# Kernel optimization log

Hardware: AMD Instinct MI355X
Metric: run time of the kernel (lower is better)

## Reference

```python
import jax, jax.numpy as jnp
import numpy as np

B, N, D, H, E = 4, 1024, 512, 8, 5
HD = D // H  # head_dim = 64


def _xavier(k, shape):
    fan_out, fan_in = shape
    s = (2.0 / (fan_in + fan_out)) ** 0.5
    return jax.random.normal(k, shape, jnp.float32) * s


def setup_inputs() -> dict:
    key = jax.random.key(0)
    ks = jax.random.split(key, 7)
    x = jax.random.normal(ks[0], (B, N, D), jnp.float32)
    edge_features = jax.random.normal(ks[1], (B, N, N, E), jnp.float32)
    node_mask = jax.random.randint(ks[2], (B, N), 0, 2).astype(bool)
    w_qkv = _xavier(ks[3], (3 * D, D))
    w_ep = _xavier(ks[4], (H, E))
    w_eg = _xavier(ks[5], (H, E))
    b_eg = jnp.zeros((H,), jnp.float32)
    w_proj = _xavier(ks[6], (D, D))
    b_proj = jnp.zeros((D,), jnp.float32)
    return {"x": x, "edge_features": edge_features, "node_mask": node_mask,
            "w_qkv": w_qkv, "w_ep": w_ep, "w_eg": w_eg, "b_eg": b_eg,
            "w_proj": w_proj, "b_proj": b_proj}


def reference(x, edge_features, node_mask, w_qkv, w_ep, w_eg, b_eg, w_proj, b_proj):
    b, n, d = x.shape
    scale = HD ** -0.5
    # qkv projection (torch Linear: y = x @ W^T), split into q,k,v (b,H,n,HD)
    qkv = (x @ w_qkv.T).reshape(b, n, 3, H, HD)
    qkv = jnp.transpose(qkv, (2, 0, 3, 1, 4))
    q, k, v = qkv[0], qkv[1], qkv[2]
    # attention scores (b,H,n,n)
    scores = jnp.einsum('bhnd,bhmd->bhnm', q, k) * scale
    # edge bias and sigmoid gate, (b,n,n,E) @ (E,H) -> (b,H,n,n)
    edge_bias = jnp.einsum('bnme,he->bhnm', edge_features, w_ep)
    edge_gates = jax.nn.sigmoid(
        jnp.einsum('bnme,he->bhnm', edge_features, w_eg) + b_eg[None, :, None, None])
    scores = scores + edge_gates * edge_bias
    # pairwise valid mask, broadcast over heads
    m = node_mask[:, None, :, None] & node_mask[:, None, None, :]  # (b,1,n,n)
    scores = jnp.where(m, scores, -jnp.inf)
    row_valid = jnp.any(m, axis=-1)  # (b,1,n)
    scores = jnp.where(row_valid[..., None], scores, 0.0)
    attn = jax.nn.softmax(scores, axis=-1)
    out = jnp.einsum('bhnm,bhmd->bhnd', attn, v)
    out = jnp.transpose(out, (0, 2, 1, 3)).reshape(b, n, d)
    return out @ w_proj.T + b_proj
```

## Files before the change

kernel.cpp:

```cpp
#include <hip/hip_runtime.h>
#include <hip/hip_bf16.h>

#define Bb 4
#define Nn 1024
#define Dd 512
#define Hh 8
#define Ee 5
#define HDd 64

typedef unsigned int u32_t;
typedef unsigned short u16_t;
typedef short s16x8 __attribute__((ext_vector_type(8)));
typedef float f32x4 __attribute__((ext_vector_type(4)));

#define MFMA(a, b, c) __builtin_amdgcn_mfma_f32_16x16x32_bf16((a), (b), (c), 0, 0, 0)

__device__ __forceinline__ u32_t pack32(float x) {
    u32_t u = __float_as_uint(x);
    u32_t hi = u & 0xffff0000u;
    float rem = x - __uint_as_float(hi);
    u32_t r = __float_as_uint(rem);
    u32_t lo = (r + 0x7fffu + ((r >> 16) & 1u)) >> 16;
    return hi | (lo & 0xffffu);
}

__device__ __forceinline__ void unpk8(uint4 A, uint4 B, s16x8& h, s16x8& l) {
    union { u16_t u[8]; s16x8 v; } H, L;
    u32_t a[8] = {A.x, A.y, A.z, A.w, B.x, B.y, B.z, B.w};
    #pragma unroll
    for (int i = 0; i < 8; i++) { H.u[i] = (u16_t)(a[i] >> 16); L.u[i] = (u16_t)(a[i] & 0xffffu); }
    h = H.v; l = L.v;
}

__device__ __forceinline__ void split4(uint4 A, uint2& hi, uint2& lo) {
    hi.x = (A.x >> 16) | (A.y & 0xffff0000u);
    hi.y = (A.z >> 16) | (A.w & 0xffff0000u);
    lo.x = (A.x & 0xffffu) | (A.y << 16);
    lo.y = (A.z & 0xffffu) | (A.w << 16);
}

__global__ __launch_bounds__(256) void prep_mask(const void* __restrict__ msk,
                                                 int* __restrict__ mw,
                                                 int* __restrict__ anyB) {
    __shared__ int notint;
    __shared__ int ab[Bb];
    const int tid = threadIdx.x;
    if (tid == 0) notint = 0;
    if (tid < Bb) ab[tid] = 0;
    __syncthreads();
    const u32_t* wp = (const u32_t*)msk;
    int bad = 0;
    for (int i = tid; i < 1024; i += 256) bad |= (wp[i] > 1u);
    if (bad) atomicOr(&notint, 1);
    __syncthreads();
    const int isbyte = notint;
    const unsigned char* bp = (const unsigned char*)msk;
    for (int i = tid; i < Bb * Nn; i += 256) {
        const int v = isbyte ? (bp[i] != 0) : (wp[i] != 0);
        mw[i] = v;
        if (v) atomicOr(&ab[i >> 10], 1);
    }
    __syncthreads();
    if (tid < Bb) anyB[tid] = ab[tid];
}

__global__ __launch_bounds__(256) void pack3(const float* __restrict__ x,
                                             const float* __restrict__ wq,
                                             const float* __restrict__ wpj,
                                             u32_t* __restrict__ xp,
                                             u32_t* __restrict__ wqp,
                                             u32_t* __restrict__ wpp) {
    const int gt = blockIdx.x * 256 + threadIdx.x;
    const int gs = gridDim.x * 256;
    const float4* xs = (const float4*)x;
    uint4* xd = (uint4*)xp;
    for (int i = gt; i < (Bb * Nn * Dd) / 4; i += gs) {
        float4 v = xs[i];
        xd[i] = make_uint4(pack32(v.x), pack32(v.y), pack32(v.z), pack32(v.w));
    }
    const float4* qs = (const float4*)wq;
    uint4* qd = (uint4*)wqp;
    for (int i = gt; i < (3 * Dd * Dd) / 4; i += gs) {
        float4 v = qs[i];
        qd[i] = make_uint4(pack32(v.x), pack32(v.y), pack32(v.z), pack32(v.w));
    }
    const float4* ps = (const float4*)wpj;
    uint4* pd = (uint4*)wpp;
    for (int i = gt; i < (Dd * Dd) / 4; i += gs) {
        float4 v = ps[i];
        pd[i] = make_uint4(pack32(v.x), pack32(v.y), pack32(v.z), pack32(v.w));
    }
}

__global__ __launch_bounds__(256) void qkv_mfma(const u32_t* __restrict__ xp,
                                                const u32_t* __restrict__ wp,
                                                u32_t* __restrict__ q32,
                                                u32_t* __restrict__ k32,
                                                u32_t* __restrict__ v32) {
    __shared__ __align__(16) u16_t Xh[64 * 72], Xl[64 * 72];
    __shared__ __align__(16) u16_t Wh[64 * 72], Wl[64 * 72];
    const int tid = threadIdx.x;
    const int wv = tid >> 6, lane = tid & 63, lm = lane & 15, quad = lane >> 4;
    const int m0 = blockIdx.y * 64, c0 = blockIdx.x * 64;
    const int row = tid >> 2, dq = tid & 3;
    const uint4* x4 = (const uint4*)xp;
    const uint4* w4 = (const uint4*)wp;

    f32x4 acc[4];
    #pragma unroll
    for (int nt = 0; nt < 4; nt++) acc[nt] = {0.f, 0.f, 0.f, 0.f};

    for (int kt = 0; kt < 8; kt++) {
        __syncthreads();
        #pragma unroll
        for (int t = 0; t < 4; t++) {
            const int cc = dq * 4 + t;
            uint4 A = x4[(size_t)(m0 + row) * 128 + kt * 16 + cc];
            uint2 hi, lo;
            split4(A, hi, lo);
            *(uint2*)&Xh[row * 72 + cc * 4] = hi;
            *(uint2*)&Xl[row * 72 + cc * 4] = lo;
            uint4 Bv = w4[(size_t)(c0 + row) * 128 + kt * 16 + cc];
            split4(Bv, hi, lo);
            *(uint2*)&Wh[row * 72 + cc * 4] = hi;
            *(uint2*)&Wl[row * 72 + cc * 4] = lo;
        }
        __syncthreads();
        s16x8 ah[2], al[2];
        #pragma unroll
        for (int ks = 0; ks < 2; ks++) {
            ah[ks] = *(const s16x8*)&Xh[(16 * wv + lm) * 72 + ks * 32 + quad * 8];
            al[ks] = *(const s16x8*)&Xl[(16 * wv + lm) * 72 + ks * 32 + quad * 8];
        }
        #pragma unroll
        for (int nt = 0; nt < 4; nt++) {
            #pragma unroll
            for (int ks = 0; ks < 2; ks++) {
                s16x8 bh = *(const s16x8*)&Wh[(16 * nt + lm) * 72 + ks * 32 + quad * 8];
                s16x8 bl = *(const s16x8*)&Wl[(16 * nt + lm) * 72 + ks * 32 + quad * 8];
                acc[nt] = MFMA(ah[ks], bh, acc[nt]);
                acc[nt] = MFMA(ah[ks], bl, acc[nt]);
                acc[nt] = MFMA(al[ks], bh, acc[nt]);
            }
        }
    }
    #pragma unroll
    for (int nt = 0; nt < 4; nt++) {
        const int c = c0 + 16 * nt + lm;
        const int s = c >> 9, hd = c & 511, h = hd >> 6, d = hd & 63;
        u32_t* dst = (s == 0) ? q32 : (s == 1) ? k32 : v32;
        #pragma unroll
        for (int r = 0; r < 4; r++) {
            const int m = m0 + 16 * wv + 4 * quad + r;
            const int b = m >> 10, n = m & (Nn - 1);
            dst[(((size_t)b * Hh + h) * Nn + n) * HDd + d] = pack32(acc[nt][r]);
        }
    }
}

__global__ __launch_bounds__(256, 2) void attn_mfma(const u32_t* __restrict__ q32,
                                                    const u32_t* __restrict__ k32,
                                                    const u32_t* __restrict__ v32,
                                                    const float* __restrict__ ef,
                                                    const int* __restrict__ mw,
                                                    const int* __restrict__ anyB,
                                                    const float* __restrict__ wep,
                                                    const float* __restrict__ weg,
                                                    const float* __restrict__ beg,
                                                    u32_t* __restrict__ aoutp) {
    __shared__ __align__(16) u16_t Qh[64 * 72], Ql[64 * 72];
    __shared__ __align__(16) char KP[18432];
    __shared__ __align__(16) u16_t VTh[64 * 88], VTl[64 * 88];
    u16_t* Kh = (u16_t*)KP;
    u16_t* Kl = Kh + 64 * 72;
    u32_t* Ppk = (u32_t*)KP;

    const int tid = threadIdx.x;
    const int wv = tid >> 6, lane = tid & 63, lm = lane & 15, quad = lane >> 4;
    const int i0 = blockIdx.x * 64;
    const int h  = blockIdx.y;
    const int b  = blockIdx.z;

    const float wp0 = wep[h*Ee+0], wp1 = wep[h*Ee+1], wp2 = wep[h*Ee+2],
                wp3 = wep[h*Ee+3], wp4 = wep[h*Ee+4];
    const float wg0 = weg[h*Ee+0], wg1 = weg[h*Ee+1], wg2 = weg[h*Ee+2],
                wg3 = weg[h*Ee+3], wg4 = weg[h*Ee+4];
    const float bgs = beg[h];

    const uint4* qg4 = (const uint4*)(q32 + (((size_t)b * Hh + h) * Nn + i0) * HDd);
    const uint4* kg4 = (const uint4*)(k32 + (((size_t)b * Hh + h) * Nn) * HDd);
    const uint4* vg4 = (const uint4*)(v32 + (((size_t)b * Hh + h) * Nn) * HDd);
    const int* mwB = mw + b * Nn;

    {
        const int row = tid >> 2, dq = tid & 3;
        #pragma unroll
        for (int t = 0; t < 4; t++) {
            const int cc = dq * 4 + t;
            uint4 A = qg4[row * 16 + cc];
            uint2 hi, lo;
            split4(A, hi, lo);
            *(uint2*)&Qh[row * 72 + cc * 4] = hi;
            *(uint2*)&Ql[row * 72 + cc * 4] = lo;
        }
    }

    const int anyb = anyB[b];
    int rv[4];
    float m_[4], l_[4];
    f32x4 accO[4];
    const float* efrow[4];
    #pragma unroll
    for (int r = 0; r < 4; r++) {
        const int i = i0 + 16 * wv + 4 * quad + r;
        rv[r] = anyb && mwB[i];
        m_[r] = -1e30f; l_[r] = 0.f;
        efrow[r] = ef + ((size_t)(b * Nn + i) * Nn + lm) * Ee;
    }
    #pragma unroll
    for (int dn = 0; dn < 4; dn++) accO[dn] = {0.f, 0.f, 0.f, 0.f};

    for (int jt = 0; jt < Nn / 64; jt++) {
        const int j0 = jt * 64;

        int mj[4];
        #pragma unroll
        for (int jn = 0; jn < 4; jn++) mj[jn] = mwB[j0 + 16 * jn + lm];
        float er[4][4][5];
        #pragma unroll
        for (int r = 0; r < 4; r++) {
            const float* pr = efrow[r] + (size_t)j0 * Ee;
            #pragma unroll
            for (int jn = 0; jn < 4; jn++) {
                #pragma unroll
                for (int e = 0; e < 5; e++) er[r][jn][e] = pr[jn * (16 * Ee) + e];
            }
        }

        __syncthreads();

        {
            const int row = tid >> 2, dq = tid & 3;
            #pragma unroll
            for (int t = 0; t < 4; t++) {
                const int cc = dq * 4 + t;
                uint4 A = kg4[(j0 + row) * 16 + cc];
                uint2 hi, lo;
                split4(A, hi, lo);
                *(uint2*)&Kh[row * 72 + cc * 4] = hi;
                *(uint2*)&Kl[row * 72 + cc * 4] = lo;
            }
        }
        {
            const int jg = tid >> 4, dc = tid & 15;
            u32_t r0[4], r1[4], r2[4], r3[4];
            uint4 A0 = vg4[(j0 + 4 * jg + 0) * 16 + dc];
            uint4 A1 = vg4[(j0 + 4 * jg + 1) * 16 + dc];
            uint4 A2 = vg4[(j0 + 4 * jg + 2) * 16 + dc];
            uint4 A3 = vg4[(j0 + 4 * jg + 3) * 16 + dc];
            r0[0]=A0.x; r0[1]=A0.y; r0[2]=A0.z; r0[3]=A0.w;
            r1[0]=A1.x; r1[1]=A1.y; r1[2]=A1.z; r1[3]=A1.w;
            r2[0]=A2.x; r2[1]=A2.y; r2[2]=A2.z; r2[3]=A2.w;
            r3[0]=A3.x; r3[1]=A3.y; r3[2]=A3.z; r3[3]=A3.w;
            #pragma unroll
            for (int c = 0; c < 4; c++) {
                const int d = 4 * dc + c;
                uint2 hi, lo;
                hi.x = (r0[c] >> 16) | (r1[c] & 0xffff0000u);
                hi.y = (r2[c] >> 16) | (r3[c] & 0xffff0000u);
                lo.x = (r0[c] & 0xffffu) | (r1[c] << 16);
                lo.y = (r2[c] & 0xffffu) | (r3[c] << 16);
                *(uint2*)&VTh[d * 88 + 4 * jg] = hi;
                *(uint2*)&VTl[d * 88 + 4 * jg] = lo;
            }
        }
        __syncthreads();

        s16x8 qh[2], ql[2];
        #pragma unroll
        for (int ks = 0; ks < 2; ks++) {
            qh[ks] = *(const s16x8*)&Qh[(16 * wv + lm) * 72 + ks * 32 + quad * 8];
            ql[ks] = *(const s16x8*)&Ql[(16 * wv + lm) * 72 + ks * 32 + quad * 8];
        }
        f32x4 S[4];
        #pragma unroll
        for (int jn = 0; jn < 4; jn++) {
            f32x4 s = {0.f, 0.f, 0.f, 0.f};
            #pragma unroll
            for (int ks = 0; ks < 2; ks++) {
                s16x8 bh = *(const s16x8*)&Kh[(16 * jn + lm) * 72 + ks * 32 + quad * 8];
                s16x8 bl = *(const s16x8*)&Kl[(16 * jn + lm) * 72 + ks * 32 + quad * 8];
                s = MFMA(qh[ks], bh, s);
                s = MFMA(qh[ks], bl, s);
                s = MFMA(ql[ks], bh, s);
            }
            S[jn] = s;
        }

        float pv[4][4];
        #pragma unroll
        for (int r = 0; r < 4; r++) {
            float sv[4];
            #pragma unroll
            for (int jn = 0; jn < 4; jn++) {
                const float e0 = er[r][jn][0], e1 = er[r][jn][1], e2 = er[r][jn][2],
                            e3 = er[r][jn][3], e4 = er[r][jn][4];
                const float bias = fmaf(e0, wp0, fmaf(e1, wp1, fmaf(e2, wp2, fmaf(e3, wp3, e4 * wp4))));
                const float gv = fmaf(e0, wg0, fmaf(e1, wg1, fmaf(e2, wg2, fmaf(e3, wg3, fmaf(e4, wg4, bgs)))));
                const float gate = __builtin_amdgcn_rcpf(1.f + __expf(-gv));
                const float val = fmaf(S[jn][r], 0.125f, gate * bias);
                sv[jn] = rv[r] ? (mj[jn] ? val : -1e30f) : 0.f;
            }
            float tmax = fmaxf(fmaxf(sv[0], sv[1]), fmaxf(sv[2], sv[3]));
            tmax = fmaxf(tmax, __shfl_xor(tmax, 1));
            tmax = fmaxf(tmax, __shfl_xor(tmax, 2));
            tmax = fmaxf(tmax, __shfl_xor(tmax, 4));
            tmax = fmaxf(tmax, __shfl_xor(tmax, 8));
            const float mnew = fmaxf(m_[r], tmax);
            const float alpha = __expf(m_[r] - mnew);
            float ps = 0.f;
            #pragma unroll
            for (int jn = 0; jn < 4; jn++) { pv[r][jn] = __expf(sv[jn] - mnew); ps += pv[r][jn]; }
            ps += __shfl_xor(ps, 1);
            ps += __shfl_xor(ps, 2);
            ps += __shfl_xor(ps, 4);
            ps += __shfl_xor(ps, 8);
            m_[r] = mnew;
            l_[r] = l_[r] * alpha + ps;
            #pragma unroll
            for (int dn = 0; dn < 4; dn++) accO[dn][r] *= alpha;
        }

        __syncthreads();
        #pragma unroll
        for (int r = 0; r < 4; r++)
            #pragma unroll
            for (int jn = 0; jn < 4; jn++)
                Ppk[(16 * wv + 4 * quad + r) * 68 + 16 * jn + lm] = pack32(pv[r][jn]);

        s16x8 ph[2], pl[2];
        #pragma unroll
        for (int ks2 = 0; ks2 < 2; ks2++) {
            const int off = (16 * wv + lm) * 68 + ks2 * 32 + quad * 8;
            uint4 A = *(const uint4*)&Ppk[off];
            uint4 B = *(const uint4*)&Ppk[off + 4];
            unpk8(A, B, ph[ks2], pl[ks2]);
        }
        #pragma unroll
        for (int dn = 0; dn < 4; dn++) {
            f32x4 c = accO[dn];
            #pragma unroll
            for (int ks2 = 0; ks2 < 2; ks2++) {
                s16x8 vh = *(const s16x8*)&VTh[(16 * dn + lm) * 88 + ks2 * 32 + quad * 8];
                s16x8 vl = *(const s16x8*)&VTl[(16 * dn + lm) * 88 + ks2 * 32 + quad * 8];
                c = MFMA(ph[ks2], vh, c);
                c = MFMA(ph[ks2], vl, c);
                c = MFMA(pl[ks2], vh, c);
            }
            accO[dn] = c;
        }
    }

    #pragma unroll
    for (int r = 0; r < 4; r++) {
        const int i = i0 + 16 * wv + 4 * quad + r;
        const float inv = __builtin_amdgcn_rcpf(l_[r]);
        #pragma unroll
        for (int dn = 0; dn < 4; dn++)
            aoutp[(size_t)(b * Nn + i) * Dd + h * HDd + 16 * dn + lm] = pack32(accO[dn][r] * inv);
    }
}

__global__ __launch_bounds__(256) void out_mfma(const u32_t* __restrict__ ap,
                                                const u32_t* __restrict__ wp,
                                                const float* __restrict__ bias,
                                                float* __restrict__ out) {
    __shared__ __align__(16) u16_t Xh[64 * 72], Xl[64 * 72];
    __shared__ __align__(16) u16_t Wh[64 * 72], Wl[64 * 72];
    const int tid = threadIdx.x;
    const int wv = tid >> 6, lane = tid & 63, lm = lane & 15, quad = lane >> 4;
    const int m0 = blockIdx.y * 64, c0 = blockIdx.x * 64;
    const int row = tid >> 2, dq = tid & 3;
    const uint4* a4 = (const uint4*)ap;
    const uint4* w4 = (const uint4*)wp;

    f32x4 acc[4];
    #pragma unroll
    for (int nt = 0; nt < 4; nt++) acc[nt] = {0.f, 0.f, 0.f, 0.f};

    for (int kt = 0; kt < 8; kt++) {
        __syncthreads();
        #pragma unroll
        for (int t = 0; t < 4; t++) {
            const int cc = dq * 4 + t;
            uint4 A = a4[(size_t)(m0 + row) * 128 + kt * 16 + cc];
            uint2 hi, lo;
            split4(A, hi, lo);
            *(uint2*)&Xh[row * 72 + cc * 4] = hi;
            *(uint2*)&Xl[row * 72 + cc * 4] = lo;
            uint4 Bv = w4[(size_t)(c0 + row) * 128 + kt * 16 + cc];
            split4(Bv, hi, lo);
            *(uint2*)&Wh[row * 72 + cc * 4] = hi;
            *(uint2*)&Wl[row * 72 + cc * 4] = lo;
        }
        __syncthreads();
        s16x8 ah[2], al[2];
        #pragma unroll
        for (int ks = 0; ks < 2; ks++) {
            ah[ks] = *(const s16x8*)&Xh[(16 * wv + lm) * 72 + ks * 32 + quad * 8];
            al[ks] = *(const s16x8*)&Xl[(16 * wv + lm) * 72 + ks * 32 + quad * 8];
        }
        #pragma unroll
        for (int nt = 0; nt < 4; nt++) {
            #pragma unroll
            for (int ks = 0; ks < 2; ks++) {
                s16x8 bh = *(const s16x8*)&Wh[(16 * nt + lm) * 72 + ks * 32 + quad * 8];
                s16x8 bl = *(const s16x8*)&Wl[(16 * nt + lm) * 72 + ks * 32 + quad * 8];
                acc[nt] = MFMA(ah[ks], bh, acc[nt]);
                acc[nt] = MFMA(ah[ks], bl, acc[nt]);
                acc[nt] = MFMA(al[ks], bh, acc[nt]);
            }
        }
    }
    #pragma unroll
    for (int nt = 0; nt < 4; nt++) {
        const int c = c0 + 16 * nt + lm;
        const float bc = bias[c];
        #pragma unroll
        for (int r = 0; r < 4; r++) {
            const int m = m0 + 16 * wv + 4 * quad + r;
            out[(size_t)m * Dd + c] = acc[nt][r] + bc;
        }
    }
}

extern "C" void kernel_launch(void* const* d_in, const int* in_sizes, int n_in,
                              void* d_out, int out_size, void* d_ws, size_t ws_size,
                              hipStream_t stream) {
    const float* x    = (const float*)d_in[0];
    const float* ef   = (const float*)d_in[1];
    const void*  msk  = d_in[2];
    const float* wqkv = (const float*)d_in[3];
    const float* wep  = (const float*)d_in[4];
    const float* weg  = (const float*)d_in[5];
    const float* beg  = (const float*)d_in[6];
    const float* wpj  = (const float*)d_in[7];
    const float* bpj  = (const float*)d_in[8];
    float* out = (float*)d_out;

    int* mw   = (int*)d_ws;
    int* anyB = mw + Bb * Nn;
    u32_t* q32 = (u32_t*)(anyB + 16);
    const size_t per = (size_t)Bb * Hh * Nn * HDd;
    u32_t* k32 = q32 + per;
    u32_t* v32 = k32 + per;
    u32_t* aop = v32 + per;
    u32_t* xp  = aop + (size_t)Bb * Nn * Dd;
    u32_t* wqp = xp + (size_t)Bb * Nn * Dd;
    u32_t* wpp = wqp + (size_t)3 * Dd * Dd;

    prep_mask<<<1, 256, 0, stream>>>(msk, mw, anyB);
    pack3<<<1024, 256, 0, stream>>>(x, wqkv, wpj, xp, wqp, wpp);
    qkv_mfma<<<dim3(24, 64), 256, 0, stream>>>(xp, wqp, q32, k32, v32);
    attn_mfma<<<dim3(Nn / 64, Hh, Bb), 256, 0, stream>>>(q32, k32, v32, ef, mw, anyB,
                                                         wep, weg, beg, aop);
    out_mfma<<<dim3(8, 64), 256, 0, stream>>>(aop, wpp, bpj, out);
}
```

Before: 310.9 us.

## Transpose score MFMA so edge features load as contiguous float4 per lane

The attention kernel now computes K·Qᵀ instead of Q·Kᵀ. Each lane then owns one query row and four consecutive key columns, so the edge-feature reads become contiguous float4 loads and the softmax row reductions run across quads instead of across 16 lanes. The P buffer gets its own XOR-swizzled shared-memory region, which removes one __syncthreads per tile at the cost of more LDS. Q fragments are hoisted out of the loop, and the staging loops in all three kernels use wider 16-byte LDS stores.

```diff
diff --git a/kernel.cpp b/kernel.cpp
--- a/kernel.cpp
+++ b/kernel.cpp
@@ -37,6 +37,16 @@
     hi.y = (A.z >> 16) | (A.w & 0xffff0000u);
     lo.x = (A.x & 0xffffu) | (A.y << 16);
     lo.y = (A.z & 0xffffu) | (A.w << 16);
+}
+
+__device__ __forceinline__ void stage16(uint4 A0, uint4 A1, uint4 A2, uint4 A3,
+                                        u16_t* dh, u16_t* dl) {
+    uint2 h0, l0, h1, l1, h2, l2, h3, l3;
+    split4(A0, h0, l0); split4(A1, h1, l1); split4(A2, h2, l2); split4(A3, h3, l3);
+    *(uint4*)(dh + 0) = make_uint4(h0.x, h0.y, h1.x, h1.y);
+    *(uint4*)(dh + 8) = make_uint4(h2.x, h2.y, h3.x, h3.y);
+    *(uint4*)(dl + 0) = make_uint4(l0.x, l0.y, l1.x, l1.y);
+    *(uint4*)(dl + 8) = make_uint4(l2.x, l2.y, l3.x, l3.y);
 }
 
 __global__ __launch_bounds__(256) void prep_mask(const void* __restrict__ msk,
@@ -112,18 +122,13 @@
 
     for (int kt = 0; kt < 8; kt++) {
         __syncthreads();
-        #pragma unroll
-        for (int t = 0; t < 4; t++) {
-            const int cc = dq * 4 + t;
-            uint4 A = x4[(size_t)(m0 + row) * 128 + kt * 16 + cc];
-            uint2 hi, lo;
-            split4(A, hi, lo);
-            *(uint2*)&Xh[row * 72 + cc * 4] = hi;
-            *(uint2*)&Xl[row * 72 + cc * 4] = lo;
-            uint4 Bv = w4[(size_t)(c0 + row) * 128 + kt * 16 + cc];
-            split4(Bv, hi, lo);
-            *(uint2*)&Wh[row * 72 + cc * 4] = hi;
-            *(uint2*)&Wl[row * 72 + cc * 4] = lo;
+        {
+            const size_t xb = (size_t)(m0 + row) * 128 + kt * 16 + dq * 4;
+            stage16(x4[xb + 0], x4[xb + 1], x4[xb + 2], x4[xb + 3],
+                    &Xh[row * 72 + dq * 16], &Xl[row * 72 + dq * 16]);
+            const size_t wb = (size_t)(c0 + row) * 128 + kt * 16 + dq * 4;
+            stage16(w4[wb + 0], w4[wb + 1], w4[wb + 2], w4[wb + 3],
+                    &Wh[row * 72 + dq * 16], &Wl[row * 72 + dq * 16]);
         }
         __syncthreads();
         s16x8 ah[2], al[2];
@@ -169,11 +174,9 @@
                                                     const float* __restrict__ beg,
                                                     u32_t* __restrict__ aoutp) {
     __shared__ __align__(16) u16_t Qh[64 * 72], Ql[64 * 72];
-    __shared__ __align__(16) char KP[18432];
+    __shared__ __align__(16) u16_t Kh[64 * 72], Kl[64 * 72];
     __shared__ __align__(16) u16_t VTh[64 * 88], VTl[64 * 88];
-    u16_t* Kh = (u16_t*)KP;
-    u16_t* Kl = Kh + 64 * 72;
-    u32_t* Ppk = (u32_t*)KP;
+    __shared__ __align__(16) u32_t Ppk[64 * 68];
 
     const int tid = threadIdx.x;
     const int wv = tid >> 6, lane = tid & 63, lm = lane & 15, quad = lane >> 4;
@@ -194,65 +197,51 @@
 
     {
         const int row = tid >> 2, dq = tid & 3;
-        #pragma unroll
-        for (int t = 0; t < 4; t++) {
-            const int cc = dq * 4 + t;
-            uint4 A = qg4[row * 16 + cc];
-            uint2 hi, lo;
-            split4(A, hi, lo);
-            *(uint2*)&Qh[row * 72 + cc * 4] = hi;
-            *(uint2*)&Ql[row * 72 + cc * 4] = lo;
-        }
+        const size_t qb = (size_t)row * 16 + dq * 4;
+        stage16(qg4[qb + 0], qg4[qb + 1], qg4[qb + 2], qg4[qb + 3],
+                &Qh[row * 72 + dq * 16], &Ql[row * 72 + dq * 16]);
+    }
+    __syncthreads();
+    s16x8 qh[2], ql[2];
+    #pragma unroll
+    for (int ks = 0; ks < 2; ks++) {
+        qh[ks] = *(const s16x8*)&Qh[(16 * wv + lm) * 72 + ks * 32 + quad * 8];
+        ql[ks] = *(const s16x8*)&Ql[(16 * wv + lm) * 72 + ks * 32 + quad * 8];
     }
 
     const int anyb = anyB[b];
-    int rv[4];
-    float m_[4], l_[4];
+    const int i_sm = i0 + 16 * wv + lm;
+    const int rvs = anyb && mwB[i_sm];
+    float m_ = -1e30f, l_ = 0.f;
     f32x4 accO[4];
-    const float* efrow[4];
-    #pragma unroll
-    for (int r = 0; r < 4; r++) {
-        const int i = i0 + 16 * wv + 4 * quad + r;
-        rv[r] = anyb && mwB[i];
-        m_[r] = -1e30f; l_[r] = 0.f;
-        efrow[r] = ef + ((size_t)(b * Nn + i) * Nn + lm) * Ee;
-    }
     #pragma unroll
     for (int dn = 0; dn < 4; dn++) accO[dn] = {0.f, 0.f, 0.f, 0.f};
+    const float* efL = ef + ((size_t)(b * Nn + i_sm) * Nn + 4 * quad) * Ee;
+    const int xk = 8 * (lm & 3);
 
     for (int jt = 0; jt < Nn / 64; jt++) {
         const int j0 = jt * 64;
 
-        int mj[4];
-        #pragma unroll
-        for (int jn = 0; jn < 4; jn++) mj[jn] = mwB[j0 + 16 * jn + lm];
-        float er[4][4][5];
-        #pragma unroll
-        for (int r = 0; r < 4; r++) {
-            const float* pr = efrow[r] + (size_t)j0 * Ee;
-            #pragma unroll
-            for (int jn = 0; jn < 4; jn++) {
-                #pragma unroll
-                for (int e = 0; e < 5; e++) er[r][jn][e] = pr[jn * (16 * Ee) + e];
-            }
+        int4 mj4[4];
+        float4 er4[4][5];
+        #pragma unroll
+        for (int jn = 0; jn < 4; jn++) {
+            mj4[jn] = *(const int4*)&mwB[j0 + 16 * jn + 4 * quad];
+            const float4* p4 = (const float4*)(efL + (size_t)(j0 + 16 * jn) * Ee);
+            #pragma unroll
+            for (int c = 0; c < 5; c++) er4[jn][c] = p4[c];
         }
 
         __syncthreads();
 
         {
             const int row = tid >> 2, dq = tid & 3;
-            #pragma unroll
-            for (int t = 0; t < 4; t++) {
-                const int cc = dq * 4 + t;
-                uint4 A = kg4[(j0 + row) * 16 + cc];
-                uint2 hi, lo;
-                split4(A, hi, lo);
-                *(uint2*)&Kh[row * 72 + cc * 4] = hi;
-                *(uint2*)&Kl[row * 72 + cc * 4] = lo;
-            }
+            const size_t kb = (size_t)(j0 + row) * 16 + dq * 4;
+            stage16(kg4[kb + 0], kg4[kb + 1], kg4[kb + 2], kg4[kb + 3],
+                    &Kh[row * 72 + dq * 16], &Kl[row * 72 + dq * 16]);
         }
         {
-            const int jg = tid >> 4, dc = tid & 15;
+            const int jg = tid & 15, dc = tid >> 4;
             u32_t r0[4], r1[4], r2[4], r3[4];
             uint4 A0 = vg4[(j0 + 4 * jg + 0) * 16 + dc];
             uint4 A1 = vg4[(j0 + 4 * jg + 1) * 16 + dc];
@@ -276,75 +265,83 @@
         }
         __syncthreads();
 
-        s16x8 qh[2], ql[2];
-        #pragma unroll
-        for (int ks = 0; ks < 2; ks++) {
-            qh[ks] = *(const s16x8*)&Qh[(16 * wv + lm) * 72 + ks * 32 + quad * 8];
-            ql[ks] = *(const s16x8*)&Ql[(16 * wv + lm) * 72 + ks * 32 + quad * 8];
-        }
-        f32x4 S[4];
+        f32x4 Sp[4];
         #pragma unroll
         for (int jn = 0; jn < 4; jn++) {
             f32x4 s = {0.f, 0.f, 0.f, 0.f};
             #pragma unroll
             for (int ks = 0; ks < 2; ks++) {
-                s16x8 bh = *(const s16x8*)&Kh[(16 * jn + lm) * 72 + ks * 32 + quad * 8];
-                s16x8 bl = *(const s16x8*)&Kl[(16 * jn + lm) * 72 + ks * 32 + quad * 8];
-                s = MFMA(qh[ks], bh, s);
-                s = MFMA(qh[ks], bl, s);
-                s = MFMA(ql[ks], bh, s);
-            }
-            S[jn] = s;
-        }
-
-        float pv[4][4];
-        #pragma unroll
-        for (int r = 0; r < 4; r++) {
-            float sv[4];
-            #pragma unroll
-            for (int jn = 0; jn < 4; jn++) {
-                const float e0 = er[r][jn][0], e1 = er[r][jn][1], e2 = er[r][jn][2],
-                            e3 = er[r][jn][3], e4 = er[r][jn][4];
+                s16x8 kh = *(const s16x8*)&Kh[(16 * jn + lm) * 72 + ks * 32 + quad * 8];
+                s16x8 kl = *(const s16x8*)&Kl[(16 * jn + lm) * 72 + ks * 32 + quad * 8];
+                s = MFMA(kh, qh[ks], s);
+                s = MFMA(kh, ql[ks], s);
+                s = MFMA(kl, qh[ks], s);
+            }
+            Sp[jn] = s;
+        }
+
+        float pp[4][4];
+        #pragma unroll
+        for (int jn = 0; jn < 4; jn++) {
+            const int mjv[4] = {mj4[jn].x, mj4[jn].y, mj4[jn].z, mj4[jn].w};
+            #pragma unroll
+            for (int r = 0; r < 4; r++) {
+                const int f = r * 5;
+                const float e0 = er4[jn][(f+0)>>2][(f+0)&3];
+                const float e1 = er4[jn][(f+1)>>2][(f+1)&3];
+                const float e2 = er4[jn][(f+2)>>2][(f+2)&3];
+                const float e3 = er4[jn][(f+3)>>2][(f+3)&3];
+                const float e4 = er4[jn][(f+4)>>2][(f+4)&3];
                 const float bias = fmaf(e0, wp0, fmaf(e1, wp1, fmaf(e2, wp2, fmaf(e3, wp3, e4 * wp4))));
                 const float gv = fmaf(e0, wg0, fmaf(e1, wg1, fmaf(e2, wg2, fmaf(e3, wg3, fmaf(e4, wg4, bgs)))));
                 const float gate = __builtin_amdgcn_rcpf(1.f + __expf(-gv));
-                const float val = fmaf(S[jn][r], 0.125f, gate * bias);
-                sv[jn] = rv[r] ? (mj[jn] ? val : -1e30f) : 0.f;
-            }
-            float tmax = fmaxf(fmaxf(sv[0], sv[1]), fmaxf(sv[2], sv[3]));
-            tmax = fmaxf(tmax, __shfl_xor(tmax, 1));
-            tmax = fmaxf(tmax, __shfl_xor(tmax, 2));
-            tmax = fmaxf(tmax, __shfl_xor(tmax, 4));
-            tmax = fmaxf(tmax, __shfl_xor(tmax, 8));
-            const float mnew = fmaxf(m_[r], tmax);
-            const float alpha = __expf(m_[r] - mnew);
-            float ps = 0.f;
-            #pragma unroll
-            for (int jn = 0; jn < 4; jn++) { pv[r][jn] = __expf(sv[jn] - mnew); ps += pv[r][jn]; }
-            ps += __shfl_xor(ps, 1);
-            ps += __shfl_xor(ps, 2);
-            ps += __shfl_xor(ps, 4);
-            ps += __shfl_xor(ps, 8);
-            m_[r] = mnew;
-            l_[r] = l_[r] * alpha + ps;
-            #pragma unroll
-            for (int dn = 0; dn < 4; dn++) accO[dn][r] *= alpha;
-        }
-
-        __syncthreads();
-        #pragma unroll
-        for (int r = 0; r < 4; r++)
-            #pragma unroll
-            for (int jn = 0; jn < 4; jn++)
-                Ppk[(16 * wv + 4 * quad + r) * 68 + 16 * jn + lm] = pack32(pv[r][jn]);
+                const float val = fmaf(Sp[jn][r], 0.125f, gate * bias);
+                pp[jn][r] = rvs ? (mjv[r] ? val : -1e30f) : 0.f;
+            }
+        }
+        float tmax = fmaxf(fmaxf(fmaxf(pp[0][0], pp[0][1]), fmaxf(pp[0][2], pp[0][3])),
+                           fmaxf(fmaxf(pp[1][0], pp[1][1]), fmaxf(pp[1][2], pp[1][3])));
+        tmax = fmaxf(tmax,
+               fmaxf(fmaxf(fmaxf(pp[2][0], pp[2][1]), fmaxf(pp[2][2], pp[2][3])),
+                     fmaxf(fmaxf(pp[3][0], pp[3][1]), fmaxf(pp[3][2], pp[3][3]))));
+        tmax = fmaxf(tmax, __shfl_xor(tmax, 16));
+        tmax = fmaxf(tmax, __shfl_xor(tmax, 32));
+        const float mnew = fmaxf(m_, tmax);
+        const float alpha = __expf(m_ - mnew);
+        float ps = 0.f;
+        #pragma unroll
+        for (int jn = 0; jn < 4; jn++)
+            #pragma unroll
+            for (int r = 0; r < 4; r++) { pp[jn][r] = __expf(pp[jn][r] - mnew); ps += pp[jn][r]; }
+        ps += __shfl_xor(ps, 16);
+        ps += __shfl_xor(ps, 32);
+        m_ = mnew;
+        l_ = l_ * alpha + ps;
+        float a4[4];
+        #pragma unroll
+        for (int r = 0; r < 4; r++) a4[r] = __shfl(alpha, 4 * quad + r);
+        #pragma unroll
+        for (int dn = 0; dn < 4; dn++)
+            #pragma unroll
+            for (int r = 0; r < 4; r++) accO[dn][r] *= a4[r];
+
+        #pragma unroll
+        for (int jn = 0; jn < 4; jn++) {
+            #pragma unroll
+            for (int p = 0; p < 2; p++) {
+                const int col = (16 * jn + 4 * quad + 2 * p) ^ xk;
+                *(uint2*)&Ppk[(16 * wv + lm) * 68 + col] =
+                    make_uint2(pack32(pp[jn][2 * p]), pack32(pp[jn][2 * p + 1]));
+            }
+        }
 
         s16x8 ph[2], pl[2];
         #pragma unroll
         for (int ks2 = 0; ks2 < 2; ks2++) {
-            const int off = (16 * wv + lm) * 68 + ks2 * 32 + quad * 8;
+            const int off = (16 * wv + lm) * 68 + ((ks2 * 32 + quad * 8) ^ xk);
             uint4 A = *(const uint4*)&Ppk[off];
-            uint4 B = *(const uint4*)&Ppk[off + 4];
-            unpk8(A, B, ph[ks2], pl[ks2]);
+            uint4 B2 = *(const uint4*)&Ppk[off + 4];
+            unpk8(A, B2, ph[ks2], pl[ks2]);
         }
         #pragma unroll
         for (int dn = 0; dn < 4; dn++) {
@@ -361,13 +358,15 @@
         }
     }
 
+    float linv[4];
+    #pragma unroll
+    for (int r = 0; r < 4; r++) linv[r] = __builtin_amdgcn_rcpf(__shfl(l_, 4 * quad + r));
     #pragma unroll
     for (int r = 0; r < 4; r++) {
         const int i = i0 + 16 * wv + 4 * quad + r;
-        const float inv = __builtin_amdgcn_rcpf(l_[r]);
         #pragma unroll
         for (int dn = 0; dn < 4; dn++)
-            aoutp[(size_t)(b * Nn + i) * Dd + h * HDd + 16 * dn + lm] = pack32(accO[dn][r] * inv);
+            aoutp[(size_t)(b * Nn + i) * Dd + h * HDd + 16 * dn + lm] = pack32(accO[dn][r] * linv[r]);
     }
 }
 
@@ -390,18 +389,13 @@
 
     for (int kt = 0; kt < 8; kt++) {
         __syncthreads();
-        #pragma unroll
-        for (int t = 0; t < 4; t++) {
-            const int cc = dq * 4 + t;
-            uint4 A = a4[(size_t)(m0 + row) * 128 + kt * 16 + cc];
-            uint2 hi, lo;
-            split4(A, hi, lo);
-            *(uint2*)&Xh[row * 72 + cc * 4] = hi;
-            *(uint2*)&Xl[row * 72 + cc * 4] = lo;
-            uint4 Bv = w4[(size_t)(c0 + row) * 128 + kt * 16 + cc];
-            split4(Bv, hi, lo);
-            *(uint2*)&Wh[row * 72 + cc * 4] = hi;
-            *(uint2*)&Wl[row * 72 + cc * 4] = lo;
+        {
+            const size_t ab = (size_t)(m0 + row) * 128 + kt * 16 + dq * 4;
+            stage16(a4[ab + 0], a4[ab + 1], a4[ab + 2], a4[ab + 3],
+                    &Xh[row * 72 + dq * 16], &Xl[row * 72 + dq * 16]);
+            const size_t wb = (size_t)(c0 + row) * 128 + kt * 16 + dq * 4;
+            stage16(w4[wb + 0], w4[wb + 1], w4[wb + 2], w4[wb + 3],
+                    &Wh[row * 72 + dq * 16], &Wl[row * 72 + dq * 16]);
         }
         __syncthreads();
         s16x8 ah[2], al[2];
```

New measurement: 335.2 us. 1.08x slower.
